# Kernel optimization log

Measured on AMD Instinct MI355X. Metric: run time of the kernel, lower is better.

The kernel has to match this reference:

```python
import jax, jax.numpy as jnp
import numpy as np

N = 25000      # nodes
E = 400000     # edges (before self-loops)
F_IN = 128     # num_node_features
HID = 16       # hidden_channels
HEADS = 12     # GAT heads
OUT = 32       # output_channels


def setup_inputs() -> dict:
    key = jax.random.key(0)
    ks = jax.random.split(key, 16)
    def glorot(k, shape):
        fan_in = shape[0]
        return jax.random.normal(k, shape, jnp.float32) / np.sqrt(fan_in)
    return {
        "x": jax.random.normal(ks[0], (N, 1, F_IN), jnp.float32),
        "edge_index": jax.random.randint(ks[1], (2, E), 0, N, jnp.int64),
        # GCNConv 1
        "W1": glorot(ks[2], (F_IN, HID)),
        "b1": jnp.zeros((HID,), jnp.float32),
        # GATConv (heads=12, concat)
        "Wg": glorot(ks[3], (HID, HEADS * HID)),
        "att_src": jax.random.normal(ks[4], (HEADS, HID), jnp.float32) * 0.1,
        "att_dst": jax.random.normal(ks[5], (HEADS, HID), jnp.float32) * 0.1,
        "bg": jnp.zeros((HEADS * HID,), jnp.float32),
        # GCNConv 2 and 3
        "W2": glorot(ks[6], (HEADS * HID, HID)),
        "b2": jnp.zeros((HID,), jnp.float32),
        "W3": glorot(ks[7], (HID, HID)),
        "b3": jnp.zeros((HID,), jnp.float32),
        # final Linear
        "Wlin": glorot(ks[8], (HID, OUT)),
        "blin": jnp.zeros((OUT,), jnp.float32),
    }


def _add_self_loops(edge_index, n):
    loop = jnp.arange(n, dtype=edge_index.dtype)
    src = jnp.concatenate([edge_index[0], loop])
    dst = jnp.concatenate([edge_index[1], loop])
    return src, dst


def _gcn_conv(x, W, b, src, dst, n):
    # PyG GCNConv: symmetric normalization with self-loops (already in src/dst)
    h = x @ W                                            # [N, C]
    deg = jax.ops.segment_sum(jnp.ones_like(dst, jnp.float32), dst, n)
    dinv = jnp.where(deg > 0, jax.lax.rsqrt(deg), 0.0)   # deg^-0.5
    norm = dinv[src] * dinv[dst]                         # [E']
    out = jax.ops.segment_sum(h[src] * norm[:, None], dst, n)
    return out + b


def _gat_conv(x, Wg, att_src, att_dst, bg, src, dst, n):
    # PyG GATConv, concat=True, negative_slope=0.2, self-loops in src/dst
    h = (x @ Wg).reshape(n, HEADS, HID)                  # [N, H, C]
    a_s = jnp.sum(h * att_src, axis=-1)                  # [N, H]
    a_d = jnp.sum(h * att_dst, axis=-1)                  # [N, H]
    e = a_s[src] + a_d[dst]                              # [E', H]
    e = jnp.where(e > 0, e, 0.2 * e)                     # leaky_relu
    m = jax.ops.segment_max(e, dst, n)                   # stable softmax per dst
    ex = jnp.exp(e - m[dst])
    denom = jax.ops.segment_sum(ex, dst, n)
    alpha = ex / denom[dst]                              # [E', H]
    out = jax.ops.segment_sum(alpha[:, :, None] * h[src], dst, n)  # [N, H, C]
    return out.reshape(n, HEADS * HID) + bg


def reference(x, edge_index, W1, b1, Wg, att_src, att_dst, bg, W2, b2, W3, b3, Wlin, blin):
    n = x.shape[0]
    src, dst = _add_self_loops(edge_index, n)
    xs = x.squeeze(1)                                    # [N, F]
    x1 = jax.nn.relu(_gcn_conv(xs, W1, b1, src, dst, n))
    # dropout p=0.5 is identity in eval mode
    x2 = jax.nn.elu(_gat_conv(x1, Wg, att_src, att_dst, bg, src, dst, n))
    x3 = jax.nn.relu(_gcn_conv(x2, W2, b2, src, dst, n))
    x4 = jax.nn.relu(_gcn_conv(x3, W3, b3, src, dst, n)) + x3
    x4 = jnp.mean(x4, axis=0, keepdims=True)             # [1, HID]
    return x4 @ Wlin + blin                              # [1, OUT]
```

## Files before the change

kernel.cpp:

```cpp
#include <hip/hip_runtime.h>

#define F_IN 128
#define HID 16
#define HEADS 12
#define HF (HEADS*HID)
#define OUT_C 32

__global__ void k_detect(const int* __restrict__ ei, int E, int* __restrict__ flag) {
    __shared__ int sacc[256];
    int t = threadIdx.x;
    long long half = (long long)E;
    int acc = 0;
    #pragma unroll
    for (int i = 0; i < 8; i++) {
        long long k = ((long long)(t + i * 256) * half) / 2048;
        acc |= ei[2 * k + 1];
    }
    sacc[t] = acc;
    __syncthreads();
    for (int off = 128; off >= 1; off >>= 1) {
        if (t < off) sacc[t] |= sacc[t + off];
        __syncthreads();
    }
    if (t == 0) flag[1] = sacc[0];
}

__global__ void k_convert(const void* __restrict__ ei, int E, const int* __restrict__ flag,
                          int* __restrict__ src32, int* __restrict__ dst32,
                          int* __restrict__ count) {
    int e = blockIdx.x * blockDim.x + threadIdx.x;
    if (e >= E) return;
    int s, d;
    if (flag[1] == 0) {
        const long long* p = (const long long*)ei;
        s = (int)p[e];
        d = (int)p[(size_t)E + e];
    } else {
        const int* p = (const int*)ei;
        s = p[e];
        d = p[(size_t)E + e];
    }
    src32[e] = s;
    dst32[e] = d;
    atomicAdd(&count[d], 1);
}


__global__ void k_scan(const int* __restrict__ count, int* __restrict__ rowstart,
                       float* __restrict__ dinv, int n) {
    __shared__ int part[1024];
    int t = threadIdx.x;
    int chunk = (n + 1023) >> 10;
    int beg = t * chunk;
    int end = beg + chunk; if (end > n) end = n;
    int s = 0;
    for (int i = beg; i < end; i++) s += count[i];
    part[t] = s;
    __syncthreads();
    for (int off = 1; off < 1024; off <<= 1) {
        int v = (t >= off) ? part[t - off] : 0;
        __syncthreads();
        part[t] += v;
        __syncthreads();
    }
    int run = (t == 0) ? 0 : part[t - 1];
    for (int i = beg; i < end; i++) {
        rowstart[i] = run;
        int c = count[i];
        run += c;
        dinv[i] = rsqrtf((float)(c + 1));
    }
    if (t == 1023) rowstart[n] = run;
}

__global__ void k_fill(const int* __restrict__ srcA, const int* __restrict__ dstA, int E,
                       const int* __restrict__ rowstart, int* __restrict__ cursor,
                       int* __restrict__ csr) {
    int e = blockIdx.x * blockDim.x + threadIdx.x;
    if (e < E) {
        int d = dstA[e];
        int p = atomicAdd(&cursor[d], 1);
        csr[rowstart[d] + p] = srcA[e];
    }
}


__global__ void k_gemm1(const float* __restrict__ x, const float* __restrict__ W,
                        float* __restrict__ h, int n) {
    __shared__ float sW[F_IN * HID];
    __shared__ float sX[16][F_IN + 1];
    int t = threadIdx.x;
    for (int i = t; i < F_IN * HID; i += 256) sW[i] = W[i];
    int node0 = blockIdx.x * 16;
    for (int i = t; i < 16 * F_IN; i += 256) {
        int r = i >> 7, c = i & 127;
        int node = node0 + r;
        sX[r][c] = (node < n) ? x[node * F_IN + c] : 0.f;
    }
    __syncthreads();
    int ln = t >> 4, c = t & 15;
    float acc = 0.f;
    #pragma unroll 8
    for (int k = 0; k < F_IN; k++) acc += sX[ln][k] * sW[k * HID + c];
    int node = node0 + ln;
    if (node < n) h[node * HID + c] = acc;
}

__global__ void k_gemm_gat(const float* __restrict__ x1, const float* __restrict__ Wg,
                           const float* __restrict__ att_s, const float* __restrict__ att_d,
                           float* __restrict__ hg, float* __restrict__ a_s,
                           float* __restrict__ a_d, int n) {
    int c = threadIdx.x;
    int lane = c & 63;
    int hh = c >> 4, ci = c & 15;
    float ats = att_s[c];
    float atd = att_d[c];
    float wcol[HID];
    #pragma unroll
    for (int k = 0; k < HID; k++) wcol[k] = Wg[k * HF + c];
    for (int node = blockIdx.x; node < n; node += gridDim.x) {
        float xv = x1[node * HID + (lane & 15)];
        float acc = 0.f;
        #pragma unroll
        for (int k = 0; k < HID; k++) acc += __shfl(xv, k) * wcol[k];
        hg[(size_t)node * HF + c] = acc;
        float vs = acc * ats, vd = acc * atd;
        #pragma unroll
        for (int msk = 8; msk >= 1; msk >>= 1) {
            vs += __shfl_xor(vs, msk);
            vd += __shfl_xor(vd, msk);
        }
        if (ci == 0) {
            a_s[node * HEADS + hh] = vs;
            a_d[node * HEADS + hh] = vd;
        }
    }
}


__global__ void k_gcn_agg(const float* __restrict__ h, const int* __restrict__ rowstart,
                          const int* __restrict__ csr, const float* __restrict__ dinv,
                          const float* __restrict__ bias, const float* __restrict__ resid,
                          float* __restrict__ out, int n) {
    int node = (blockIdx.x * blockDim.x + threadIdx.x) >> 6;
    int lane = threadIdx.x & 63;
    if (node >= n) return;
    int c = lane & 15, jj = lane >> 4;
    float dn = dinv[node];
    int base = rowstart[node], deg = rowstart[node + 1] - base;
    float acc = (jj == 0) ? h[node * HID + c] * dn : 0.f;
    int j = jj;
    for (; j + 4 < deg; j += 8) {
        int s0 = csr[base + j], s1 = csr[base + j + 4];
        float d0 = dinv[s0], d1 = dinv[s1];
        float h0 = h[s0 * HID + c], h1 = h[s1 * HID + c];
        acc += h0 * d0 + h1 * d1;
    }
    if (j < deg) {
        int s0 = csr[base + j];
        acc += h[s0 * HID + c] * dinv[s0];
    }
    acc += __shfl_xor(acc, 16);
    acc += __shfl_xor(acc, 32);
    if (lane < 16) {
        float v = fmaxf(acc * dn + bias[c], 0.f);
        if (resid) v += resid[node * HID + c];
        out[node * HID + c] = v;
    }
}

__global__ void k_gcn_agg_f3(const float* __restrict__ h, const int* __restrict__ rowstart,
                             const int* __restrict__ csr, const float* __restrict__ dinv,
                             const float* __restrict__ bias, const float* __restrict__ W3,
                             float* __restrict__ x3o, float* __restrict__ h3o, int n) {
    int node = (blockIdx.x * blockDim.x + threadIdx.x) >> 6;
    int lane = threadIdx.x & 63;
    if (node >= n) return;
    int c = lane & 15, jj = lane >> 4;
    float dn = dinv[node];
    int base = rowstart[node], deg = rowstart[node + 1] - base;
    float acc = (jj == 0) ? h[node * HID + c] * dn : 0.f;
    int j = jj;
    for (; j + 4 < deg; j += 8) {
        int s0 = csr[base + j], s1 = csr[base + j + 4];
        float d0 = dinv[s0], d1 = dinv[s1];
        float h0 = h[s0 * HID + c], h1 = h[s1 * HID + c];
        acc += h0 * d0 + h1 * d1;
    }
    if (j < deg) {
        int s0 = csr[base + j];
        acc += h[s0 * HID + c] * dinv[s0];
    }
    acc += __shfl_xor(acc, 16);
    acc += __shfl_xor(acc, 32);
    float v = fmaxf(acc * dn + bias[c], 0.f);
    if (lane < 16) x3o[node * HID + c] = v;
    int gbase = lane & 48;
    float hacc = 0.f;
    #pragma unroll
    for (int cc = 0; cc < 16; cc++)
        hacc += __shfl(v, gbase | cc) * W3[cc * HID + c];
    if (lane < 16) h3o[node * HID + c] = hacc;
}

__global__ void k_gat_agg(const float* __restrict__ hg, const float* __restrict__ a_s,
                          const float* __restrict__ a_d, const int* __restrict__ rowstart,
                          const int* __restrict__ csr, const float* __restrict__ bg,
                          const float* __restrict__ W2, float* __restrict__ h2, int n) {
    int node = (blockIdx.x * blockDim.x + threadIdx.x) >> 6;
    int lane = threadIdx.x & 63;
    if (node >= n) return;
    int base = rowstart[node], deg = rowstart[node + 1] - base;
    int dcap = deg < 64 ? deg : 64;
    int eidx = (lane < dcap) ? csr[base + lane] : 0;

    int hA = lane % 12;
    int hh0 = lane >> 4;
    int hh1 = (lane + 64) >> 4;
    int hh2 = (lane + 128) >> 4;

    float adA = a_d[node * HEADS + hA];
    float e0 = a_s[node * HEADS + hA] + adA;
    e0 = (e0 > 0.f) ? e0 : 0.2f * e0;
    float m = e0, s = 1.f;
    float acc0 = hg[(size_t)node * HF + lane];
    float acc1 = hg[(size_t)node * HF + lane + 64];
    float acc2 = hg[(size_t)node * HF + lane + 128];

#define GAT_EDGE(AS, G0, G1, G2)                                      \
    {                                                                 \
        float e = (AS) + adA;                                         \
        e = (e > 0.f) ? e : 0.2f * e;                                 \
        float d = e - m;                                              \
        float p = __expf(d);                                          \
        if (__any(d > 8.f)) {                       \
            bool big = d > 8.f;                                       \
            float rp = big ? __expf(-d) : 1.f;                        \
            float pe = big ? 1.f : p;                                 \
            s = s * rp + pe;                                          \
            if (big) m = e;                                           \
            acc0 = acc0 * __shfl(rp, hh0) + __shfl(pe, hh0) * (G0);   \
            acc1 = acc1 * __shfl(rp, hh1) + __shfl(pe, hh1) * (G1);   \
            acc2 = acc2 * __shfl(rp, hh2) + __shfl(pe, hh2) * (G2);   \
        } else {                                                      \
            s += p;                                                   \
            acc0 += __shfl(p, hh0) * (G0);                            \
            acc1 += __shfl(p, hh1) * (G1);                            \
            acc2 += __shfl(p, hh2) * (G2);                            \
        }                                                             \
    }

    int j = 0;
    for (; j + 4 <= dcap; j += 4) {
        int s0 = __shfl(eidx, j),     s1 = __shfl(eidx, j + 1);
        int s2 = __shfl(eidx, j + 2), s3 = __shfl(eidx, j + 3);
        float A0 = a_s[s0 * HEADS + hA], A1 = a_s[s1 * HEADS + hA];
        float A2 = a_s[s2 * HEADS + hA], A3 = a_s[s3 * HEADS + hA];
        float g00 = hg[(size_t)s0 * HF + lane], g01 = hg[(size_t)s0 * HF + lane + 64], g02 = hg[(size_t)s0 * HF + lane + 128];
        float g10 = hg[(size_t)s1 * HF + lane], g11 = hg[(size_t)s1 * HF + lane + 64], g12 = hg[(size_t)s1 * HF + lane + 128];
        float g20 = hg[(size_t)s2 * HF + lane], g21 = hg[(size_t)s2 * HF + lane + 64], g22 = hg[(size_t)s2 * HF + lane + 128];
        float g30 = hg[(size_t)s3 * HF + lane], g31 = hg[(size_t)s3 * HF + lane + 64], g32 = hg[(size_t)s3 * HF + lane + 128];
        GAT_EDGE(A0, g00, g01, g02)
        GAT_EDGE(A1, g10, g11, g12)
        GAT_EDGE(A2, g20, g21, g22)
        GAT_EDGE(A3, g30, g31, g32)
    }
    for (; j < dcap; j++) {
        int s0 = __shfl(eidx, j);
        float A0 = a_s[s0 * HEADS + hA];
        float g00 = hg[(size_t)s0 * HF + lane], g01 = hg[(size_t)s0 * HF + lane + 64], g02 = hg[(size_t)s0 * HF + lane + 128];
        GAT_EDGE(A0, g00, g01, g02)
    }
    for (; j < deg; j++) {
        int s0 = csr[base + j];
        float A0 = a_s[s0 * HEADS + hA];
        float g00 = hg[(size_t)s0 * HF + lane], g01 = hg[(size_t)s0 * HF + lane + 64], g02 = hg[(size_t)s0 * HF + lane + 128];
        GAT_EDGE(A0, g00, g01, g02)
    }
#undef GAT_EDGE

    float is = 1.f / s;
    float i0 = __shfl(is, hh0), i1 = __shfl(is, hh1), i2 = __shfl(is, hh2);
    float v0 = acc0 * i0 + bg[lane];
    float v1 = acc1 * i1 + bg[lane + 64];
    float v2 = acc2 * i2 + bg[lane + 128];
    v0 = (v0 > 0.f) ? v0 : (__expf(v0) - 1.f);
    v1 = (v1 > 0.f) ? v1 : (__expf(v1) - 1.f);
    v2 = (v2 > 0.f) ? v2 : (__expf(v2) - 1.f);

    float p[16];
    const float4* W2v = (const float4*)W2;
    #pragma unroll
    for (int q = 0; q < 4; q++) {
        float4 w0 = W2v[lane * 4 + q];
        float4 w1 = W2v[(lane + 64) * 4 + q];
        float4 w2 = W2v[(lane + 128) * 4 + q];
        p[q * 4 + 0] = v0 * w0.x + v1 * w1.x + v2 * w2.x;
        p[q * 4 + 1] = v0 * w0.y + v1 * w1.y + v2 * w2.y;
        p[q * 4 + 2] = v0 * w0.z + v1 * w1.z + v2 * w2.z;
        p[q * 4 + 3] = v0 * w0.w + v1 * w1.w + v2 * w2.w;
    }
    #pragma unroll
    for (int mask = 1; mask <= 32; mask <<= 1) {
        #pragma unroll
        for (int cq = 0; cq < 16; cq++) p[cq] += __shfl_xor(p[cq], mask);
    }
    if (lane < 16) h2[node * HID + lane] = p[lane];
}


__global__ void k_mean(const float* __restrict__ x4, float* __restrict__ red, int n) {
    __shared__ float sd[16][17];
    int t = threadIdx.x;
    int ln = t >> 4, c = t & 15;
    float acc = 0.f;
    for (int node = blockIdx.x * 16 + ln; node < n; node += gridDim.x * 16)
        acc += x4[node * HID + c];
    sd[ln][c] = acc;
    __syncthreads();
    for (int off = 8; off >= 1; off >>= 1) {
        if (ln < off) sd[ln][c] += sd[ln + off][c];
        __syncthreads();
    }
    if (ln == 0) atomicAdd(&red[c], sd[0][c]);
}

__global__ void k_final(const float* __restrict__ red, const float* __restrict__ Wlin,
                        const float* __restrict__ blin, float* __restrict__ out, float invN) {
    int o = threadIdx.x;
    if (o >= OUT_C) return;
    float acc = blin[o];
    #pragma unroll
    for (int c = 0; c < HID; c++) acc += (red[c] * invN) * Wlin[c * OUT_C + o];
    out[o] = acc;
}


extern "C" void kernel_launch(void* const* d_in, const int* in_sizes, int n_in,
                              void* d_out, int out_size, void* d_ws, size_t ws_size,
                              hipStream_t stream) {
    const float* x     = (const float*)d_in[0];
    const void*  ei    = d_in[1];
    const float* W1    = (const float*)d_in[2];
    const float* b1    = (const float*)d_in[3];
    const float* Wg    = (const float*)d_in[4];
    const float* att_s = (const float*)d_in[5];
    const float* att_d = (const float*)d_in[6];
    const float* bg    = (const float*)d_in[7];
    const float* W2    = (const float*)d_in[8];
    const float* b2    = (const float*)d_in[9];
    const float* W3    = (const float*)d_in[10];
    const float* b3    = (const float*)d_in[11];
    const float* Wlin  = (const float*)d_in[12];
    const float* blin  = (const float*)d_in[13];
    float* out = (float*)d_out;

    int N = in_sizes[0] / F_IN;
    int E = in_sizes[1] / 2;

    char* w = (char*)d_ws;
    size_t off = 0;
    auto alloc = [&](size_t bytes) -> void* {
        void* p = w + off;
        off += (bytes + 255) & ~(size_t)255;
        return p;
    };
    int*   flag     = (int*)alloc(256);
    int*   count    = (int*)alloc((size_t)N * 4);
    int*   cursor   = (int*)alloc((size_t)N * 4);
    float* red      = (float*)alloc(64);
    size_t zbytes   = (size_t)((char*)red + 256 - (char*)count);
    int*   src32    = (int*)alloc((size_t)E * 4);
    int*   dst32    = (int*)alloc((size_t)E * 4);
    int*   rowstart = (int*)alloc((size_t)(N + 1) * 4);
    int*   csr      = (int*)alloc((size_t)E * 4);
    float* dinv     = (float*)alloc((size_t)N * 4);
    float* h1       = (float*)alloc((size_t)N * HID * 4);
    float* x1       = (float*)alloc((size_t)N * HID * 4);
    float* hg       = (float*)alloc((size_t)N * HF * 4);
    float* a_s      = (float*)alloc((size_t)N * HEADS * 4);
    float* a_d      = (float*)alloc((size_t)N * HEADS * 4);
    float* h2       = (float*)alloc((size_t)N * HID * 4);
    float* x3       = (float*)alloc((size_t)N * HID * 4);
    float* h3       = (float*)alloc((size_t)N * HID * 4);
    float* x4       = (float*)alloc((size_t)N * HID * 4);
    if (off > ws_size) return;

    hipMemsetAsync(count, 0, zbytes, stream);

    int eb = (E + 255) / 256;
    int nb16 = (N + 15) / 16;
    int nbw  = (N + 3) / 4;

    k_detect<<<1, 256, 0, stream>>>((const int*)ei, E, flag);
    k_convert<<<eb, 256, 0, stream>>>(ei, E, flag, src32, dst32, count);
    k_scan<<<1, 1024, 0, stream>>>(count, rowstart, dinv, N);
    k_fill<<<eb, 256, 0, stream>>>(src32, dst32, E, rowstart, cursor, csr);

    k_gemm1<<<nb16, 256, 0, stream>>>(x, W1, h1, N);
    k_gcn_agg<<<nbw, 256, 0, stream>>>(h1, rowstart, csr, dinv, b1, nullptr, x1, N);

    k_gemm_gat<<<2048, 192, 0, stream>>>(x1, Wg, att_s, att_d, hg, a_s, a_d, N);
    k_gat_agg<<<nbw, 256, 0, stream>>>(hg, a_s, a_d, rowstart, csr, bg, W2, h2, N);

    k_gcn_agg_f3<<<nbw, 256, 0, stream>>>(h2, rowstart, csr, dinv, b2, W3, x3, h3, N);
    k_gcn_agg<<<nbw, 256, 0, stream>>>(h3, rowstart, csr, dinv, b3, x3, x4, N);

    k_mean<<<128, 256, 0, stream>>>(x4, red, N);
    k_final<<<1, 64, 0, stream>>>(red, Wlin, blin, out, 1.0f / (float)N);
}
```

Measured before the change: 316.3 us.

## Store gathered node features in fp16 and fuse mean with final linear

```diff
diff --git a/kernel.cpp b/kernel.cpp
--- a/kernel.cpp
+++ b/kernel.cpp
@@ -5,6 +5,8 @@
 #define HEADS 12
 #define HF (HEADS*HID)
 #define OUT_C 32
+
+typedef _Float16 f16;
 
 __global__ void k_detect(const int* __restrict__ ei, int E, int* __restrict__ flag) {
     __shared__ int sacc[256];
@@ -86,7 +88,7 @@
 
 
 __global__ void k_gemm1(const float* __restrict__ x, const float* __restrict__ W,
-                        float* __restrict__ h, int n) {
+                        f16* __restrict__ h, int n) {
     __shared__ float sW[F_IN * HID];
     __shared__ float sX[16][F_IN + 1];
     int t = threadIdx.x;
@@ -103,12 +105,12 @@
     #pragma unroll 8
     for (int k = 0; k < F_IN; k++) acc += sX[ln][k] * sW[k * HID + c];
     int node = node0 + ln;
-    if (node < n) h[node * HID + c] = acc;
+    if (node < n) h[node * HID + c] = (f16)acc;
 }
 
 __global__ void k_gemm_gat(const float* __restrict__ x1, const float* __restrict__ Wg,
                            const float* __restrict__ att_s, const float* __restrict__ att_d,
-                           float* __restrict__ hg, float* __restrict__ a_s,
+                           f16* __restrict__ hg, float* __restrict__ a_s,
                            float* __restrict__ a_d, int n) {
     int c = threadIdx.x;
     int lane = c & 63;
@@ -123,7 +125,7 @@
         float acc = 0.f;
         #pragma unroll
         for (int k = 0; k < HID; k++) acc += __shfl(xv, k) * wcol[k];
-        hg[(size_t)node * HF + c] = acc;
+        hg[(size_t)node * HF + c] = (f16)acc;
         float vs = acc * ats, vd = acc * atd;
         #pragma unroll
         for (int msk = 8; msk >= 1; msk >>= 1) {
@@ -138,7 +140,7 @@
 }
 
 
-__global__ void k_gcn_agg(const float* __restrict__ h, const int* __restrict__ rowstart,
+__global__ void k_gcn_agg(const f16* __restrict__ h, const int* __restrict__ rowstart,
                           const int* __restrict__ csr, const float* __restrict__ dinv,
                           const float* __restrict__ bias, const float* __restrict__ resid,
                           float* __restrict__ out, int n) {
@@ -148,17 +150,17 @@
     int c = lane & 15, jj = lane >> 4;
     float dn = dinv[node];
     int base = rowstart[node], deg = rowstart[node + 1] - base;
-    float acc = (jj == 0) ? h[node * HID + c] * dn : 0.f;
+    float acc = (jj == 0) ? (float)h[node * HID + c] * dn : 0.f;
     int j = jj;
     for (; j + 4 < deg; j += 8) {
         int s0 = csr[base + j], s1 = csr[base + j + 4];
         float d0 = dinv[s0], d1 = dinv[s1];
-        float h0 = h[s0 * HID + c], h1 = h[s1 * HID + c];
+        float h0 = (float)h[s0 * HID + c], h1 = (float)h[s1 * HID + c];
         acc += h0 * d0 + h1 * d1;
     }
     if (j < deg) {
         int s0 = csr[base + j];
-        acc += h[s0 * HID + c] * dinv[s0];
+        acc += (float)h[s0 * HID + c] * dinv[s0];
     }
     acc += __shfl_xor(acc, 16);
     acc += __shfl_xor(acc, 32);
@@ -169,27 +171,27 @@
     }
 }
 
-__global__ void k_gcn_agg_f3(const float* __restrict__ h, const int* __restrict__ rowstart,
+__global__ void k_gcn_agg_f3(const f16* __restrict__ h, const int* __restrict__ rowstart,
                              const int* __restrict__ csr, const float* __restrict__ dinv,
                              const float* __restrict__ bias, const float* __restrict__ W3,
-                             float* __restrict__ x3o, float* __restrict__ h3o, int n) {
+                             float* __restrict__ x3o, f16* __restrict__ h3o, int n) {
     int node = (blockIdx.x * blockDim.x + threadIdx.x) >> 6;
     int lane = threadIdx.x & 63;
     if (node >= n) return;
     int c = lane & 15, jj = lane >> 4;
     float dn = dinv[node];
     int base = rowstart[node], deg = rowstart[node + 1] - base;
-    float acc = (jj == 0) ? h[node * HID + c] * dn : 0.f;
+    float acc = (jj == 0) ? (float)h[node * HID + c] * dn : 0.f;
     int j = jj;
     for (; j + 4 < deg; j += 8) {
         int s0 = csr[base + j], s1 = csr[base + j + 4];
         float d0 = dinv[s0], d1 = dinv[s1];
-        float h0 = h[s0 * HID + c], h1 = h[s1 * HID + c];
+        float h0 = (float)h[s0 * HID + c], h1 = (float)h[s1 * HID + c];
         acc += h0 * d0 + h1 * d1;
     }
     if (j < deg) {
         int s0 = csr[base + j];
-        acc += h[s0 * HID + c] * dinv[s0];
+        acc += (float)h[s0 * HID + c] * dinv[s0];
     }
     acc += __shfl_xor(acc, 16);
     acc += __shfl_xor(acc, 32);
@@ -200,13 +202,13 @@
     #pragma unroll
     for (int cc = 0; cc < 16; cc++)
         hacc += __shfl(v, gbase | cc) * W3[cc * HID + c];
-    if (lane < 16) h3o[node * HID + c] = hacc;
-}
-
-__global__ void k_gat_agg(const float* __restrict__ hg, const float* __restrict__ a_s,
+    if (lane < 16) h3o[node * HID + c] = (f16)hacc;
+}
+
+__global__ void k_gat_agg(const f16* __restrict__ hg, const float* __restrict__ a_s,
                           const float* __restrict__ a_d, const int* __restrict__ rowstart,
                           const int* __restrict__ csr, const float* __restrict__ bg,
-                          const float* __restrict__ W2, float* __restrict__ h2, int n) {
+                          const float* __restrict__ W2, f16* __restrict__ h2, int n) {
     int node = (blockIdx.x * blockDim.x + threadIdx.x) >> 6;
     int lane = threadIdx.x & 63;
     if (node >= n) return;
@@ -223,9 +225,9 @@
     float e0 = a_s[node * HEADS + hA] + adA;
     e0 = (e0 > 0.f) ? e0 : 0.2f * e0;
     float m = e0, s = 1.f;
-    float acc0 = hg[(size_t)node * HF + lane];
-    float acc1 = hg[(size_t)node * HF + lane + 64];
-    float acc2 = hg[(size_t)node * HF + lane + 128];
+    float acc0 = (float)hg[(size_t)node * HF + lane];
+    float acc1 = (float)hg[(size_t)node * HF + lane + 64];
+    float acc2 = (float)hg[(size_t)node * HF + lane + 128];
 
 #define GAT_EDGE(AS, G0, G1, G2)                                      \
     {                                                                 \
@@ -256,10 +258,10 @@
         int s2 = __shfl(eidx, j + 2), s3 = __shfl(eidx, j + 3);
         float A0 = a_s[s0 * HEADS + hA], A1 = a_s[s1 * HEADS + hA];
         float A2 = a_s[s2 * HEADS + hA], A3 = a_s[s3 * HEADS + hA];
-        float g00 = hg[(size_t)s0 * HF + lane], g01 = hg[(size_t)s0 * HF + lane + 64], g02 = hg[(size_t)s0 * HF + lane + 128];
-        float g10 = hg[(size_t)s1 * HF + lane], g11 = hg[(size_t)s1 * HF + lane + 64], g12 = hg[(size_t)s1 * HF + lane + 128];
-        float g20 = hg[(size_t)s2 * HF + lane], g21 = hg[(size_t)s2 * HF + lane + 64], g22 = hg[(size_t)s2 * HF + lane + 128];
-        float g30 = hg[(size_t)s3 * HF + lane], g31 = hg[(size_t)s3 * HF + lane + 64], g32 = hg[(size_t)s3 * HF + lane + 128];
+        float g00 = (float)hg[(size_t)s0 * HF + lane], g01 = (float)hg[(size_t)s0 * HF + lane + 64], g02 = (float)hg[(size_t)s0 * HF + lane + 128];
+        float g10 = (float)hg[(size_t)s1 * HF + lane], g11 = (float)hg[(size_t)s1 * HF + lane + 64], g12 = (float)hg[(size_t)s1 * HF + lane + 128];
+        float g20 = (float)hg[(size_t)s2 * HF + lane], g21 = (float)hg[(size_t)s2 * HF + lane + 64], g22 = (float)hg[(size_t)s2 * HF + lane + 128];
+        float g30 = (float)hg[(size_t)s3 * HF + lane], g31 = (float)hg[(size_t)s3 * HF + lane + 64], g32 = (float)hg[(size_t)s3 * HF + lane + 128];
         GAT_EDGE(A0, g00, g01, g02)
         GAT_EDGE(A1, g10, g11, g12)
         GAT_EDGE(A2, g20, g21, g22)
@@ -268,13 +270,13 @@
     for (; j < dcap; j++) {
         int s0 = __shfl(eidx, j);
         float A0 = a_s[s0 * HEADS + hA];
-        float g00 = hg[(size_t)s0 * HF + lane], g01 = hg[(size_t)s0 * HF + lane + 64], g02 = hg[(size_t)s0 * HF + lane + 128];
+        float g00 = (float)hg[(size_t)s0 * HF + lane], g01 = (float)hg[(size_t)s0 * HF + lane + 64], g02 = (float)hg[(size_t)s0 * HF + lane + 128];
         GAT_EDGE(A0, g00, g01, g02)
     }
     for (; j < deg; j++) {
         int s0 = csr[base + j];
         float A0 = a_s[s0 * HEADS + hA];
-        float g00 = hg[(size_t)s0 * HF + lane], g01 = hg[(size_t)s0 * HF + lane + 64], g02 = hg[(size_t)s0 * HF + lane + 128];
+        float g00 = (float)hg[(size_t)s0 * HF + lane], g01 = (float)hg[(size_t)s0 * HF + lane + 64], g02 = (float)hg[(size_t)s0 * HF + lane + 128];
         GAT_EDGE(A0, g00, g01, g02)
     }
 #undef GAT_EDGE
@@ -305,12 +307,20 @@
         #pragma unroll
         for (int cq = 0; cq < 16; cq++) p[cq] += __shfl_xor(p[cq], mask);
     }
-    if (lane < 16) h2[node * HID + lane] = p[lane];
-}
-
-
-__global__ void k_mean(const float* __restrict__ x4, float* __restrict__ red, int n) {
+    float vout = p[0];
+    #pragma unroll
+    for (int q = 1; q < 16; q++) vout = (lane == q) ? p[q] : vout;
+    if (lane < 16) h2[node * HID + lane] = (f16)vout;
+}
+
+
+__global__ void k_mean_final(const float* __restrict__ x4, float* __restrict__ red,
+                             int* __restrict__ done, const float* __restrict__ Wlin,
+                             const float* __restrict__ blin, float* __restrict__ out,
+                             float invN, int n, int nblocks) {
     __shared__ float sd[16][17];
+    __shared__ float sred[16];
+    __shared__ int slast;
     int t = threadIdx.x;
     int ln = t >> 4, c = t & 15;
     float acc = 0.f;
@@ -323,16 +333,20 @@
         __syncthreads();
     }
     if (ln == 0) atomicAdd(&red[c], sd[0][c]);
-}
-
-__global__ void k_final(const float* __restrict__ red, const float* __restrict__ Wlin,
-                        const float* __restrict__ blin, float* __restrict__ out, float invN) {
-    int o = threadIdx.x;
-    if (o >= OUT_C) return;
-    float acc = blin[o];
-    #pragma unroll
-    for (int c = 0; c < HID; c++) acc += (red[c] * invN) * Wlin[c * OUT_C + o];
-    out[o] = acc;
+    __threadfence();
+    __syncthreads();
+    if (t == 0) slast = (atomicAdd(done, 1) == nblocks - 1);
+    __syncthreads();
+    if (slast) {
+        if (t < 16) sred[t] = atomicAdd(&red[t], 0.0f);
+        __syncthreads();
+        if (t < OUT_C) {
+            float a = blin[t];
+            #pragma unroll
+            for (int cc = 0; cc < HID; cc++) a += (sred[cc] * invN) * Wlin[cc * OUT_C + t];
+            out[t] = a;
+        }
+    }
 }
 
 
@@ -368,21 +382,22 @@
     int*   flag     = (int*)alloc(256);
     int*   count    = (int*)alloc((size_t)N * 4);
     int*   cursor   = (int*)alloc((size_t)N * 4);
-    float* red      = (float*)alloc(64);
+    float* red      = (float*)alloc(256);
+    int*   done     = (int*)((char*)red + 64);
     size_t zbytes   = (size_t)((char*)red + 256 - (char*)count);
     int*   src32    = (int*)alloc((size_t)E * 4);
     int*   dst32    = (int*)alloc((size_t)E * 4);
     int*   rowstart = (int*)alloc((size_t)(N + 1) * 4);
     int*   csr      = (int*)alloc((size_t)E * 4);
     float* dinv     = (float*)alloc((size_t)N * 4);
-    float* h1       = (float*)alloc((size_t)N * HID * 4);
+    f16*   h1       = (f16*)alloc((size_t)N * HID * 2);
     float* x1       = (float*)alloc((size_t)N * HID * 4);
-    float* hg       = (float*)alloc((size_t)N * HF * 4);
+    f16*   hg       = (f16*)alloc((size_t)N * HF * 2);
     float* a_s      = (float*)alloc((size_t)N * HEADS * 4);
     float* a_d      = (float*)alloc((size_t)N * HEADS * 4);
-    float* h2       = (float*)alloc((size_t)N * HID * 4);
+    f16*   h2       = (f16*)alloc((size_t)N * HID * 2);
     float* x3       = (float*)alloc((size_t)N * HID * 4);
-    float* h3       = (float*)alloc((size_t)N * HID * 4);
+    f16*   h3       = (f16*)alloc((size_t)N * HID * 2);
     float* x4       = (float*)alloc((size_t)N * HID * 4);
     if (off > ws_size) return;
 
@@ -406,6 +421,6 @@
     k_gcn_agg_f3<<<nbw, 256, 0, stream>>>(h2, rowstart, csr, dinv, b2, W3, x3, h3, N);
     k_gcn_agg<<<nbw, 256, 0, stream>>>(h3, rowstart, csr, dinv, b3, x3, x4, N);
 
-    k_mean<<<128, 256, 0, stream>>>(x4, red, N);
-    k_final<<<1, 64, 0, stream>>>(red, Wlin, blin, out, 1.0f / (float)N);
-}
+    k_mean_final<<<128, 256, 0, stream>>>(x4, red, done, Wlin, blin, out,
+                                          1.0f / (float)N, N, 128);
+}
```

Measured after the change: 314.9 us. About the same (-0.5%).
